# Optimization experiments

Measured on AMD Instinct MI355X. Metric: run time of the kernel, lower is better.

## Reference

```python
import jax, jax.numpy as jnp
import numpy as np

N_HEAD = 16
HEAD_DIM = 64
D_MODEL = N_HEAD * HEAD_DIM  # 1024
B, L = 2, 2048

def setup_inputs() -> dict:
    key = jax.random.key(0)
    k1, k2, k3, k4, k5 = jax.random.split(key, 5)
    s = 0.02
    return {
        "hidden_states": jax.random.normal(k1, (B, L, D_MODEL), dtype=jnp.float32),
        "W_qkv": jax.random.normal(k2, (D_MODEL, 3 * D_MODEL), dtype=jnp.float32) * s,
        "b_qkv": jax.random.normal(k3, (3 * D_MODEL,), dtype=jnp.float32) * s,
        "W_proj": jax.random.normal(k4, (D_MODEL, D_MODEL), dtype=jnp.float32) * s,
        "b_proj": jax.random.normal(k5, (D_MODEL,), dtype=jnp.float32) * s,
        "window_size": 128,
    }

def reference(hidden_states, W_qkv, b_qkv, W_proj, b_proj, window_size):
    Bb, Ll, Dd = hidden_states.shape
    # GPT-2 Conv1D: x @ W + b
    qkv = hidden_states @ W_qkv + b_qkv  # [B, L, 3D]
    q, k, v = jnp.split(qkv, 3, axis=2)
    def to_heads(t):
        return t.reshape(Bb, Ll, N_HEAD, HEAD_DIM).transpose(0, 2, 1, 3)  # [B,H,L,d]
    q, k, v = to_heads(q), to_heads(k), to_heads(v)
    scale = jnp.sqrt(jnp.asarray(HEAD_DIM, dtype=q.dtype))
    scores = jnp.einsum('bhqd,bhkd->bhqk', q, k) / scale  # [B,H,L,L]
    pos = jnp.arange(Ll)
    dist = pos[:, None] - pos[None, :]  # query - key
    sw_mask = (dist < 0) | (dist >= window_size)  # True = masked out
    scores = jnp.where(sw_mask[None, None, :, :], jnp.asarray(-jnp.inf, scores.dtype), scores)
    attn_weights = jax.nn.softmax(scores, axis=-1)  # dropout is identity (eval)
    out = jnp.einsum('bhqk,bhkd->bhqd', attn_weights, v)  # [B,H,L,d]
    out = out.transpose(0, 2, 1, 3).reshape(Bb, Ll, Dd)
    out = out @ W_proj + b_proj
    return (out, attn_weights)
```

## Files before the change

### kernel.cpp

```cpp
#include <hip/hip_runtime.h>
#include <stdint.h>

#define NH 16
#define HD 64
#define DM 1024
#define BB 2
#define LL 2048

typedef __bf16 bf16x8 __attribute__((ext_vector_type(8)));
typedef float f32x4 __attribute__((ext_vector_type(4)));
typedef unsigned short u16x8 __attribute__((ext_vector_type(8)));

__device__ __forceinline__ uint16_t f2bf(float f) {
  union { float f; uint32_t u; } x{f};
  uint32_t r = (x.u + 0x7fff + ((x.u >> 16) & 1)) >> 16;
  return (uint16_t)r;
}

__device__ __forceinline__ void gload_lds16(const void* g, void* l) {
  __builtin_amdgcn_global_load_lds(
      (const __attribute__((address_space(1))) unsigned int*)g,
      (__attribute__((address_space(3))) unsigned int*)l, 16, 0, 0);
}

__global__ __launch_bounds__(256) void cvt_bf16(
    const float* __restrict__ x, uint16_t* __restrict__ y, int n4) {
  int i = blockIdx.x * 256 + threadIdx.x;
  if (i >= n4) return;
  float4 v = ((const float4*)x)[i];
  ushort4 o;
  o.x = f2bf(v.x); o.y = f2bf(v.y); o.z = f2bf(v.z); o.w = f2bf(v.w);
  ((ushort4*)y)[i] = o;
}

__global__ __launch_bounds__(256) void transpose_cvt(
    const float* __restrict__ W, uint16_t* __restrict__ WT, int K, int N) {
  __shared__ float t[32][33];
  int bk = blockIdx.y * 32, bn = blockIdx.x * 32;
  int c = threadIdx.x & 31, r0 = threadIdx.x >> 5;
#pragma unroll
  for (int p = 0; p < 4; ++p) {
    int r = r0 + p * 8;
    t[r][c] = W[(size_t)(bk + r) * N + bn + c];
  }
  __syncthreads();
#pragma unroll
  for (int p = 0; p < 4; ++p) {
    int r = r0 + p * 8;
    WT[(size_t)(bn + r) * K + bk + c] = f2bf(t[c][r]);
  }
}

template <int OBF>
__global__ __launch_bounds__(256) void gemm_bt(
    const uint16_t* __restrict__ A, const uint16_t* __restrict__ BT,
    const float* __restrict__ bias, void* __restrict__ Cout,
    int M, int N, int K) {
  __shared__ uint16_t As[128 * 32];
  __shared__ uint16_t Bs[128 * 32];
  const int tid = threadIdx.x;
  const int bm = blockIdx.y * 128, bn = blockIdx.x * 128;
  const int lane = tid & 63, wave = tid >> 6;
  const int wr = wave >> 1, wc = wave & 1;
  f32x4 acc[4][4] = {};

  for (int k0 = 0; k0 < K; k0 += 32) {
#pragma unroll
    for (int c = 0; c < 2; ++c) {
      int e = c * 2048 + tid * 8;
      int r = e >> 5, col = e & 31;
      gload_lds16(A + (size_t)(bm + r) * K + k0 + col, (char*)As + (size_t)e * 2);
      gload_lds16(BT + (size_t)(bn + r) * K + k0 + col, (char*)Bs + (size_t)e * 2);
    }
    __syncthreads();

    const int kseg = (lane >> 4) * 8;
    bf16x8 af[4], bfr[4];
#pragma unroll
    for (int i = 0; i < 4; ++i)
      af[i] = *(const bf16x8*)&As[(wr * 64 + i * 16 + (lane & 15)) * 32 + kseg];
#pragma unroll
    for (int j = 0; j < 4; ++j)
      bfr[j] = *(const bf16x8*)&Bs[(wc * 64 + j * 16 + (lane & 15)) * 32 + kseg];
#pragma unroll
    for (int i = 0; i < 4; ++i)
#pragma unroll
      for (int j = 0; j < 4; ++j)
        acc[i][j] = __builtin_amdgcn_mfma_f32_16x16x32_bf16(bfr[j], af[i], acc[i][j], 0, 0, 0);
    __syncthreads();
  }

#pragma unroll
  for (int i = 0; i < 4; ++i) {
#pragma unroll
    for (int j = 0; j < 4; ++j) {
      int row = bm + wr * 64 + i * 16 + (lane & 15);
      int col = bn + wc * 64 + j * 16 + (lane >> 4) * 4;
      f32x4 bv = *(const f32x4*)&bias[col];
      f32x4 v = acc[i][j] + bv;
      if (OBF) {
        ushort4 o;
        o.x = f2bf(v[0]); o.y = f2bf(v[1]); o.z = f2bf(v[2]); o.w = f2bf(v[3]);
        *(ushort4*)&((uint16_t*)Cout)[(size_t)row * N + col] = o;
      } else {
        *(f32x4*)&((float*)Cout)[(size_t)row * N + col] = v;
      }
    }
  }
}

#define QT 32
#define KT 160
#define KS 72
#define PS 168

__global__ __launch_bounds__(256, 4) void attn_sw(
    const uint16_t* __restrict__ qkv,
    float* __restrict__ attnw,
    uint16_t* __restrict__ ctxb,
    const int* __restrict__ wsz_p) {
  __shared__ __align__(16) char smemU[KT * KS * 2];
  __shared__ __align__(16) uint16_t Qs[QT * KS];
  __shared__ __align__(16) uint16_t Psb[QT * PS];
  uint16_t* Ksb = (uint16_t*)smemU;
  float* Sf = (float*)smemU;

  const int wsz = *wsz_p;
  const int tid = threadIdx.x;
  const int lane = tid & 63, wave = tid >> 6;
  const int ntile = LL / QT;
  const int qt = blockIdx.x % ntile;
  const int h = (blockIdx.x / ntile) % NH;
  const int b = blockIdx.x / (ntile * NH);
  const int q0 = qt * QT;
  const int kmin = max(0, q0 - (wsz - 1));
  const int kbase = kmin & ~31;

  {
    int r = tid >> 3, c = (tid & 7) * 8;
    *(u16x8*)&Qs[r * KS + c] =
        *(const u16x8*)(qkv + (size_t)(b * LL + q0 + r) * (3 * DM) + h * HD + c);
  }
#pragma unroll
  for (int p = 0; p < 5; ++p) {
    int u = tid + p * 256;
    int r = u >> 3, c = (u & 7) * 8;
    *(u16x8*)&Ksb[r * KS + c] =
        *(const u16x8*)(qkv + (size_t)(b * LL + kbase + r) * (3 * DM) + DM + h * HD + c);
  }
  __syncthreads();

  const int mt = wave & 1, ntb = (wave >> 1) * 5;
  f32x4 sfrag[5];
  {
    const int kseg = (lane >> 4) * 8;
    bf16x8 aq0 = *(const bf16x8*)&Qs[(mt * 16 + (lane & 15)) * KS + kseg];
    bf16x8 aq1 = *(const bf16x8*)&Qs[(mt * 16 + (lane & 15)) * KS + 32 + kseg];
#pragma unroll
    for (int t = 0; t < 5; ++t) {
      int nt = ntb + t;
      bf16x8 bk0 = *(const bf16x8*)&Ksb[(nt * 16 + (lane & 15)) * KS + kseg];
      bf16x8 bk1 = *(const bf16x8*)&Ksb[(nt * 16 + (lane & 15)) * KS + 32 + kseg];
      f32x4 c = {0.f, 0.f, 0.f, 0.f};
      c = __builtin_amdgcn_mfma_f32_16x16x32_bf16(aq0, bk0, c, 0, 0, 0);
      c = __builtin_amdgcn_mfma_f32_16x16x32_bf16(aq1, bk1, c, 0, 0, 0);
      sfrag[t] = c;
    }
  }
  __syncthreads();

#pragma unroll
  for (int t = 0; t < 5; ++t) {
    int nt = ntb + t;
#pragma unroll
    for (int r = 0; r < 4; ++r)
      Sf[(mt * 16 + (lane >> 4) * 4 + r) * PS + nt * 16 + (lane & 15)] = sfrag[t][r];
  }
  __syncthreads();

  {
    const int qi = tid >> 3;
    const int kg = tid & 7;
    const int q = q0 + qi;
    float s[20];
#pragma unroll
    for (int j = 0; j < 20; ++j) s[j] = Sf[qi * PS + kg + 8 * j];
    float m = -1e30f;
#pragma unroll
    for (int j = 0; j < 20; ++j) {
      int gk = kbase + kg + 8 * j;
      bool valid = (gk <= q) && (gk > q - wsz);
      s[j] = valid ? s[j] * 0.125f : -1e30f;
      m = fmaxf(m, s[j]);
    }
#pragma unroll
    for (int off = 1; off < 8; off <<= 1)
      m = fmaxf(m, __shfl_xor(m, off, 64));
    float l = 0.f;
#pragma unroll
    for (int j = 0; j < 20; ++j) {
      float e = (s[j] > -1e29f) ? __expf(s[j] - m) : 0.f;
      s[j] = e;
      l += e;
    }
#pragma unroll
    for (int off = 1; off < 8; off <<= 1)
      l += __shfl_xor(l, off, 64);
    float inv = 1.f / l;
#pragma unroll
    for (int j = 0; j < 20; ++j) {
      float p = s[j] * inv;
      Sf[qi * PS + kg + 8 * j] = p;
      Psb[qi * PS + kg + 8 * j] = f2bf(p);
    }
  }
  __syncthreads();

  {
#pragma unroll
    for (int it = 0; it < 16; ++it) {
      int r = it * 2 + (tid >> 7);
      size_t rowoff = ((size_t)((b * NH + h) * LL + q0 + r)) * LL;
      int cb = (tid & 127) * 4;
#pragma unroll
      for (int jj = 0; jj < 4; ++jj) {
        int c4 = cb + jj * 512;
        f32x4 v = {0.f, 0.f, 0.f, 0.f};
        int pc = c4 - kbase;
        if (pc >= 0 && pc < KT)
          v = *(const f32x4*)&Sf[r * PS + pc];
        __builtin_nontemporal_store(v, (f32x4*)&attnw[rowoff + c4]);
      }
    }
  }

  {
    const int nt = wave;
    const int kseg = (lane >> 4) * 8;
    f32x4 ofrag[2] = {};
#pragma unroll
    for (int ks = 0; ks < 5; ++ks) {
      const uint16_t* vs = qkv + (size_t)(b * LL + kbase + ks * 32 + kseg) * (3 * DM) +
                           2 * DM + h * HD + nt * 16 + (lane & 15);
      uint16_t vb[8];
#pragma unroll
      for (int j = 0; j < 8; ++j) vb[j] = vs[(size_t)j * (3 * DM)];
      bf16x8 bv = *(const bf16x8*)vb;
#pragma unroll
      for (int m = 0; m < 2; ++m) {
        bf16x8 ap = *(const bf16x8*)&Psb[(m * 16 + (lane & 15)) * PS + ks * 32 + kseg];
        ofrag[m] = __builtin_amdgcn_mfma_f32_16x16x32_bf16(ap, bv, ofrag[m], 0, 0, 0);
      }
    }
#pragma unroll
    for (int m = 0; m < 2; ++m)
#pragma unroll
      for (int r = 0; r < 4; ++r) {
        int q = q0 + m * 16 + (lane >> 4) * 4 + r;
        ctxb[(size_t)(b * LL + q) * DM + h * HD + nt * 16 + (lane & 15)] = f2bf(ofrag[m][r]);
      }
  }
}

extern "C" void kernel_launch(void* const* d_in, const int* in_sizes, int n_in,
                              void* d_out, int out_size, void* d_ws, size_t ws_size,
                              hipStream_t stream) {
  const float* hs    = (const float*)d_in[0];
  const float* Wqkv  = (const float*)d_in[1];
  const float* bqkv  = (const float*)d_in[2];
  const float* Wproj = (const float*)d_in[3];
  const float* bproj = (const float*)d_in[4];
  const int*   wszp  = (const int*)d_in[5];

  float* out   = (float*)d_out;
  float* attnw = (float*)d_out + (size_t)BB * LL * DM;

  char* wsb = (char*)d_ws;
  uint16_t* qkv    = (uint16_t*)wsb;
  uint16_t* hsctxb = (uint16_t*)(wsb + 25165824);
  uint16_t* WqkvT  = (uint16_t*)(wsb + 25165824 + 8388608);
  uint16_t* WprojT = (uint16_t*)(wsb + 25165824 + 8388608 + 6291456);

  dim3 blk(256);

  cvt_bf16<<<dim3((BB * LL * DM / 4 + 255) / 256), blk, 0, stream>>>(hs, hsctxb, BB * LL * DM / 4);
  transpose_cvt<<<dim3(3 * DM / 32, DM / 32), blk, 0, stream>>>(Wqkv, WqkvT, DM, 3 * DM);
  transpose_cvt<<<dim3(DM / 32, DM / 32), blk, 0, stream>>>(Wproj, WprojT, DM, DM);

  gemm_bt<1><<<dim3(3 * DM / 128, BB * LL / 128), blk, 0, stream>>>(
      hsctxb, WqkvT, bqkv, (void*)qkv, BB * LL, 3 * DM, DM);

  attn_sw<<<dim3(BB * NH * (LL / QT)), blk, 0, stream>>>(qkv, attnw, hsctxb, wszp);

  gemm_bt<0><<<dim3(DM / 128, BB * LL / 128), blk, 0, stream>>>(
      hsctxb, WprojT, bproj, (void*)out, BB * LL, DM, DM);
}
```

Baseline: 657.4 us.

## Merge prep kernels into one launch and remap GEMM blocks across XCDs

Folds the hidden-state bf16 conversion and both weight transpose-converts into a single prep kernel that dispatches on block index, which removes two kernel launches. The GEMM now uses a 1D grid, and its block id is permuted so that consecutive tiles land on the same XCD (8-way interleave), aiming for better L2 reuse of A and B tiles. The remap assumes the grid count is divisible by 8 and N by 128, which holds for these fixed shapes.

```diff
diff --git a/kernel.cpp b/kernel.cpp
--- a/kernel.cpp
+++ b/kernel.cpp
@@ -23,20 +23,9 @@
       (__attribute__((address_space(3))) unsigned int*)l, 16, 0, 0);
 }
 
-__global__ __launch_bounds__(256) void cvt_bf16(
-    const float* __restrict__ x, uint16_t* __restrict__ y, int n4) {
-  int i = blockIdx.x * 256 + threadIdx.x;
-  if (i >= n4) return;
-  float4 v = ((const float4*)x)[i];
-  ushort4 o;
-  o.x = f2bf(v.x); o.y = f2bf(v.y); o.z = f2bf(v.z); o.w = f2bf(v.w);
-  ((ushort4*)y)[i] = o;
-}
-
-__global__ __launch_bounds__(256) void transpose_cvt(
-    const float* __restrict__ W, uint16_t* __restrict__ WT, int K, int N) {
-  __shared__ float t[32][33];
-  int bk = blockIdx.y * 32, bn = blockIdx.x * 32;
+__device__ __forceinline__ void transpose_tile(
+    const float* __restrict__ W, uint16_t* __restrict__ WT, int K, int N,
+    int bk, int bn, float (*t)[33]) {
   int c = threadIdx.x & 31, r0 = threadIdx.x >> 5;
 #pragma unroll
   for (int p = 0; p < 4; ++p) {
@@ -48,6 +37,29 @@
   for (int p = 0; p < 4; ++p) {
     int r = r0 + p * 8;
     WT[(size_t)(bn + r) * K + bk + c] = f2bf(t[c][r]);
+  }
+}
+
+__global__ __launch_bounds__(256) void prep(
+    const float* __restrict__ hs, uint16_t* __restrict__ hsb,
+    const float* __restrict__ Wqkv, uint16_t* __restrict__ WqkvT,
+    const float* __restrict__ Wproj, uint16_t* __restrict__ WprojT) {
+  __shared__ float t[32][33];
+  int bid = blockIdx.x;
+  if (bid < 4096) {
+    int i = bid * 256 + threadIdx.x;
+    float4 v = ((const float4*)hs)[i];
+    ushort4 o;
+    o.x = f2bf(v.x); o.y = f2bf(v.y); o.z = f2bf(v.z); o.w = f2bf(v.w);
+    ((ushort4*)hsb)[i] = o;
+  } else if (bid < 7168) {
+    int id = bid - 4096;
+    int bx = id % 96, by = id / 96;
+    transpose_tile(Wqkv, WqkvT, DM, 3 * DM, by * 32, bx * 32, t);
+  } else {
+    int id = bid - 7168;
+    int bx = id % 32, by = id / 32;
+    transpose_tile(Wproj, WprojT, DM, DM, by * 32, bx * 32, t);
   }
 }
 
@@ -59,7 +71,11 @@
   __shared__ uint16_t As[128 * 32];
   __shared__ uint16_t Bs[128 * 32];
   const int tid = threadIdx.x;
-  const int bm = blockIdx.y * 128, bn = blockIdx.x * 128;
+  const int nwg = gridDim.x;
+  int wg = blockIdx.x;
+  wg = (wg & 7) * (nwg >> 3) + (wg >> 3);
+  const int gx = N >> 7;
+  const int bm = (wg / gx) * 128, bn = (wg % gx) * 128;
   const int lane = tid & 63, wave = tid >> 6;
   const int wr = wave >> 1, wc = wave & 1;
   f32x4 acc[4][4] = {};
@@ -283,15 +299,13 @@
 
   dim3 blk(256);
 
-  cvt_bf16<<<dim3((BB * LL * DM / 4 + 255) / 256), blk, 0, stream>>>(hs, hsctxb, BB * LL * DM / 4);
-  transpose_cvt<<<dim3(3 * DM / 32, DM / 32), blk, 0, stream>>>(Wqkv, WqkvT, DM, 3 * DM);
-  transpose_cvt<<<dim3(DM / 32, DM / 32), blk, 0, stream>>>(Wproj, WprojT, DM, DM);
-
-  gemm_bt<1><<<dim3(3 * DM / 128, BB * LL / 128), blk, 0, stream>>>(
+  prep<<<dim3(8192), blk, 0, stream>>>(hs, hsctxb, Wqkv, WqkvT, Wproj, WprojT);
+
+  gemm_bt<1><<<dim3(768), blk, 0, stream>>>(
       hsctxb, WqkvT, bqkv, (void*)qkv, BB * LL, 3 * DM, DM);
 
   attn_sw<<<dim3(BB * NH * (LL / QT)), blk, 0, stream>>>(qkv, attnw, hsctxb, wszp);
 
-  gemm_bt<0><<<dim3(DM / 128, BB * LL / 128), blk, 0, stream>>>(
+  gemm_bt<0><<<dim3(256), blk, 0, stream>>>(
       hsctxb, WprojT, bproj, (void*)out, BB * LL, DM, DM);
 }
```

Result: no change. 652.4 us (-0.8%).
